# Optimization experiments

Hardware: AMD Instinct MI355X
Metric: run time of the kernel (lower is better)

Reference implementation:

```python
import jax, jax.numpy as jnp
import numpy as np

B, N = 8, 2048
IN_F, MID1, HID, MID2, OUT_F = 128, 128, 128, 128, 128
BIG = 9e15  # matches torch's 9000000000000000.0 additive mask constant


def _linear_params(key, out_d, in_d):
    # torch Linear layout: W is [out, in]
    kw, kb = jax.random.split(key)
    w = jax.random.normal(kw, (out_d, in_d), jnp.float32) * (1.0 / np.sqrt(in_d))
    b = jax.random.normal(kb, (out_d,), jnp.float32) * 0.01
    return w, b


def setup_inputs() -> dict:
    key = jax.random.key(0)
    ks = jax.random.split(key, 16)
    h = jax.random.normal(ks[0], (B, N, IN_F), jnp.float32)
    adj = jax.random.randint(ks[1], (B, N, N), 0, 2).astype(jnp.float32)
    vae2_fetures = jax.random.normal(ks[2], (B, N, OUT_F), jnp.float32)
    Wv1, bv1 = _linear_params(ks[3], MID1, IN_F)
    Wk1, bk1 = _linear_params(ks[4], MID1, IN_F)
    Wq1, bq1 = _linear_params(ks[5], MID1, IN_F)
    Wo1, bo1 = _linear_params(ks[6], HID, MID1)
    Wv2, bv2 = _linear_params(ks[7], MID2, HID)
    Wk2, bk2 = _linear_params(ks[8], MID2, HID)
    Wq2, bq2 = _linear_params(ks[9], MID2, HID)
    Wo2, bo2 = _linear_params(ks[10], OUT_F, MID2)
    Wf, bf = _linear_params(ks[11], OUT_F, 2 * OUT_F)
    return {
        "h": h, "adj": adj, "vae2_fetures": vae2_fetures,
        "Wv1": Wv1, "bv1": bv1, "Wk1": Wk1, "bk1": bk1, "Wq1": Wq1, "bq1": bq1,
        "Wo1": Wo1, "bo1": bo1,
        "Wv2": Wv2, "bv2": bv2, "Wk2": Wk2, "bk2": bk2, "Wq2": Wq2, "bq2": bq2,
        "Wo2": Wo2, "bo2": bo2, "Wf": Wf, "bf": bf,
    }


def _lin(x, W, b):
    return jnp.einsum('bnd,od->bno', x, W) + b


def _masked_att_block(x, adj, Wq, bq, Wk, bk, Wv, bv):
    v = jax.nn.relu(_lin(x, Wv, bv))          # [B,N,D]
    q = jax.nn.relu(_lin(x, Wq, bq))          # [B,N,D]
    k = jax.nn.relu(_lin(x, Wk, bk))          # [B,N,D]
    s = jnp.einsum('bnd,bmd->bnm', q, k)       # [B,N,N]
    masked = s * adj - BIG * (1.0 - adj)       # multiplicative + additive mask
    att = jax.nn.softmax(masked, axis=-1)
    return jnp.einsum('bnm,bmd->bnd', att, v)


def reference(h, adj, vae2_fetures,
              Wv1, bv1, Wk1, bk1, Wq1, bq1, Wo1, bo1,
              Wv2, bv2, Wk2, bk2, Wq2, bq2, Wo2, bo2,
              Wf, bf):
    f1 = _masked_att_block(h, adj, Wq1, bq1, Wk1, bk1, Wv1, bv1)
    f1 = _lin(f1, Wo1, bo1)                    # [B,N,HID]
    f2 = _masked_att_block(f1, adj, Wq2, bq2, Wk2, bk2, Wv2, bv2)
    f2 = _lin(f2, Wo2, bo2)                    # [B,N,OUT_F]
    f3 = jnp.concatenate([f2, vae2_fetures], axis=2)
    return _lin(f3, Wf, bf)                    # [B,N,OUT_F]
```

## Files before the change

### kernel.cpp

```cpp
#include <hip/hip_runtime.h>

typedef short s16x8 __attribute__((ext_vector_type(8)));
typedef float f32x4 __attribute__((ext_vector_type(4)));
typedef unsigned short u16x4v __attribute__((ext_vector_type(4)));

#define NSPLIT 4
#define NROWS 16384
#define MSHIFT 44.0f
#define NCH (2048 / NSPLIT / 64)

__device__ __forceinline__ unsigned short f2bf(float f) {
  union { float fl; unsigned int i; } v; v.fl = f;
  unsigned int x = v.i;
  x += 0x7fffu + ((x >> 16) & 1u);
  return (unsigned short)(x >> 16);
}
__device__ __forceinline__ s16x8 load8_bf16(const unsigned short* p) {
  return *(const s16x8*)p;
}
__device__ __forceinline__ s16x8 load8_f32(const float* p) {
  float4 a = *(const float4*)p;
  float4 b = *(const float4*)(p + 4);
  s16x8 r;
  r[0] = (short)f2bf(a.x); r[1] = (short)f2bf(a.y);
  r[2] = (short)f2bf(a.z); r[3] = (short)f2bf(a.w);
  r[4] = (short)f2bf(b.x); r[5] = (short)f2bf(b.y);
  r[6] = (short)f2bf(b.z); r[7] = (short)f2bf(b.w);
  return r;
}
__device__ __forceinline__ int vperm(int nn) {
  return (nn & ~31) | (((nn >> 2) & 3) << 3) | (((nn >> 4) & 1) << 2);
}

__device__ __forceinline__ void gload16(const void* g, void* l) {
  __builtin_amdgcn_global_load_lds(
      (const __attribute__((address_space(1))) void*)g,
      (__attribute__((address_space(3))) void*)l, 16, 0, 0);
}

__device__ __forceinline__ void pack_adj_body(
    const float* __restrict__ ADJ, unsigned long long* __restrict__ MASK)
{
  const int t = threadIdx.x;
  const int w = t >> 6;
  const int lane = t & 63;
  const int row0 = blockIdx.x * 16 + w * 4;
#pragma unroll
  for (int rr = 0; rr < 4; ++rr) {
    const float* src = ADJ + (size_t)(row0 + rr) * 2048;
    unsigned long long* dst = MASK + (size_t)(row0 + rr) * 32;
#pragma unroll 8
    for (int p = 0; p < 32; ++p) {
      const float v = src[p * 64 + lane];
      const unsigned long long word = __ballot(v != 0.f);
      if (lane == 0) dst[p] = word;
    }
  }
}

__device__ __forceinline__ void qkv_merged_body(
    const float* __restrict__ X,
    const float* __restrict__ Wq, const float* __restrict__ bq, unsigned short* __restrict__ oq,
    const float* __restrict__ Wk, const float* __restrict__ bk, unsigned short* __restrict__ ok,
    const float* __restrict__ Wv, const float* __restrict__ bv, unsigned short* __restrict__ ovt)
{
  const int t = threadIdx.x;
  const int w = t >> 6;
  const int lane = t & 63;
  const int l15 = lane & 15;
  const int quad = lane >> 4;
  const int mbase = blockIdx.x * 16;

  s16x8 a[4];
  const float* ar = X + (size_t)(mbase + l15) * 128;
#pragma unroll
  for (int ks = 0; ks < 4; ++ks) a[ks] = load8_f32(ar + ks * 32 + quad * 8);

  const float* Ws[3] = {Wq, Wk, Wv};
  const float* bs[3] = {bq, bk, bv};
  unsigned short* outs[3] = {oq, ok, ovt};

#pragma unroll
  for (int which = 0; which < 3; ++which) {
    const float* W = Ws[which];
    const float* bias = bs[which];
    unsigned short* out = outs[which];
#pragma unroll
    for (int nt = 0; nt < 2; ++nt) {
      const int n = (w * 2 + nt) * 16 + l15;
      f32x4 acc = {0.f, 0.f, 0.f, 0.f};
      const float* wr = W + (size_t)n * 128;
#pragma unroll
      for (int ks = 0; ks < 4; ++ks)
        acc = __builtin_amdgcn_mfma_f32_16x16x32_bf16(
            a[ks], load8_f32(wr + ks * 32 + quad * 8), acc, 0, 0, 0);
      const float bv_ = bias[n];
      if (which < 2) {
#pragma unroll
        for (int r = 0; r < 4; ++r)
          out[(size_t)(mbase + quad * 4 + r) * 128 + n] = f2bf(fmaxf(acc[r] + bv_, 0.f));
      } else {
        const int b  = mbase >> 11;
        const int nn = (mbase & 2047) + quad * 4;
        u16x4v pk;
#pragma unroll
        for (int r = 0; r < 4; ++r) pk[r] = f2bf(fmaxf(acc[r] + bv_, 0.f));
        *(u16x4v*)(out + (size_t)(b * 128 + n) * 2048 + vperm(nn)) = pk;
      }
    }
  }
}

__global__ __launch_bounds__(256) void qkv1_kernel(
    const float* __restrict__ x,
    const float* __restrict__ Wq, const float* __restrict__ bq, unsigned short* __restrict__ oq,
    const float* __restrict__ Wk, const float* __restrict__ bk, unsigned short* __restrict__ ok,
    const float* __restrict__ Wv, const float* __restrict__ bv, unsigned short* __restrict__ ovt,
    const float* __restrict__ adj, unsigned long long* __restrict__ mask)
{
  if (blockIdx.y == 0) qkv_merged_body(x, Wq, bq, oq, Wk, bk, ok, Wv, bv, ovt);
  else                 pack_adj_body(adj, mask);
}

__global__ __launch_bounds__(256, 2) void attn_kernel(
    const unsigned short* __restrict__ Q,
    const unsigned short* __restrict__ K,
    const unsigned short* __restrict__ VT,
    const unsigned long long* __restrict__ MASK,
    float* __restrict__ pO, float* __restrict__ pl)
{
  __shared__ __align__(16) unsigned short kbuf[2][64][128];
  __shared__ __align__(16) unsigned short vbuf[2][128][64];

  const int t = threadIdx.x;
  const int w = t >> 6;
  const int lane = t & 63;
  const int l15 = lane & 15;
  const int quad = lane >> 4;
  const int x7 = l15 & 7;

  const int gq0 = blockIdx.x * 128;
  const int b   = gq0 >> 11;
  const int wq0 = (gq0 & 2047) + w * 32;
  const int kc0 = blockIdx.y * (2048 / NSPLIT);

  const unsigned short* Kb  = K  + (size_t)(b * 2048) * 128;
  const unsigned short* VTb = VT + (size_t)(b * 128) * 2048;
  const unsigned long long* Mb = MASK + (size_t)b * 2048 * 32;

  const int krow = t >> 4;
  const int kc16 = t & 15;
  const int kchunk = kc16 ^ (krow & 7);
  const int vrow = t >> 3;
  const int vc16 = t & 7;
  const int vchunk = vc16 ^ (vrow & 7);

  s16x8 qf[2][4];
#pragma unroll
  for (int mt = 0; mt < 2; ++mt) {
    const unsigned short* qrow = Q + (size_t)(gq0 + w * 32 + mt * 16 + l15) * 128;
#pragma unroll
    for (int ks = 0; ks < 4; ++ks) qf[mt][ks] = load8_bf16(qrow + ks * 32 + quad * 8);
  }

  s16x8 ones;
#pragma unroll
  for (int i = 0; i < 8; ++i) ones[i] = (short)0x3F80;

  f32x4 accO[2][8];
  f32x4 accL[2];
#pragma unroll
  for (int mt = 0; mt < 2; ++mt) {
    accL[mt] = (f32x4){0.f, 0.f, 0.f, 0.f};
#pragma unroll
    for (int dt = 0; dt < 8; ++dt) accO[mt][dt] = (f32x4){0.f, 0.f, 0.f, 0.f};
  }

#pragma unroll
  for (int i = 0; i < 4; ++i)
    gload16(Kb + (size_t)(kc0 + i * 16 + krow) * 128 + kchunk * 8,
            &kbuf[0][i * 16 + krow][kc16 * 8]);
#pragma unroll
  for (int i = 0; i < 4; ++i)
    gload16(VTb + (size_t)(i * 32 + vrow) * 2048 + kc0 + vchunk * 8,
            &vbuf[0][i * 32 + vrow][vc16 * 8]);

  unsigned long long mwc[2];
#pragma unroll
  for (int mt = 0; mt < 2; ++mt)
    mwc[mt] = Mb[(size_t)(wq0 + mt * 16 + l15) * 32 + (kc0 >> 6)];

  __syncthreads();

#pragma unroll 2
  for (int ci = 0; ci < NCH; ++ci) {
    const int kc = kc0 + ci * 64;
    unsigned short (*kb)[128] = kbuf[ci & 1];
    unsigned short (*vb)[64]  = vbuf[ci & 1];

    if (ci + 1 < NCH) {
      unsigned short (*kbn)[128] = kbuf[(ci + 1) & 1];
      unsigned short (*vbn)[64]  = vbuf[(ci + 1) & 1];
#pragma unroll
      for (int i = 0; i < 4; ++i)
        gload16(Kb + (size_t)(kc + 64 + i * 16 + krow) * 128 + kchunk * 8,
                &kbn[i * 16 + krow][kc16 * 8]);
#pragma unroll
      for (int i = 0; i < 4; ++i)
        gload16(VTb + (size_t)(i * 32 + vrow) * 2048 + (kc + 64) + vchunk * 8,
                &vbn[i * 32 + vrow][vc16 * 8]);
    }

    unsigned long long kept[2];
    kept[0] = mwc[0];
    kept[1] = mwc[1];
    if (ci + 1 < NCH) {
#pragma unroll
      for (int mt = 0; mt < 2; ++mt)
        mwc[mt] = Mb[(size_t)(wq0 + mt * 16 + l15) * 32 + ((kc + 64) >> 6)];
    }

    f32x4 sv[2][4];
#pragma unroll
    for (int nt = 0; nt < 4; ++nt) {
      sv[0][nt] = (f32x4){0.f, 0.f, 0.f, 0.f};
      sv[1][nt] = (f32x4){0.f, 0.f, 0.f, 0.f};
    }
    __builtin_amdgcn_s_setprio(1);
#pragma unroll
    for (int nt = 0; nt < 4; ++nt)
#pragma unroll
      for (int ks = 0; ks < 4; ++ks) {
        s16x8 kf = *(const s16x8*)&kb[nt * 16 + l15][((ks * 4 + quad) ^ x7) * 8];
        sv[0][nt] = __builtin_amdgcn_mfma_f32_16x16x32_bf16(kf, qf[0][ks], sv[0][nt], 0, 0, 0);
        sv[1][nt] = __builtin_amdgcn_mfma_f32_16x16x32_bf16(kf, qf[1][ks], sv[1][nt], 0, 0, 0);
      }
    __builtin_amdgcn_s_setprio(0);

    s16x8 pf[2][2];
#pragma unroll
    for (int mt = 0; mt < 2; ++mt) {
      const unsigned int bl = (unsigned int)(kept[mt] >> (quad * 4));
      const unsigned int bh = (unsigned int)(kept[mt] >> (quad * 4 + 32));
#pragma unroll
      for (int ks = 0; ks < 2; ++ks) {
        s16x8 v;
#pragma unroll
        for (int half = 0; half < 2; ++half) {
          const int nt = ks * 2 + half;
          const unsigned int bits = (nt < 2) ? bl : bh;
          const int sh = (nt & 1) * 16;
#pragma unroll
          for (int r = 0; r < 4; ++r) {
            const float e = __expf(sv[mt][nt][r] - MSHIFT);
            const bool keep = (bits >> (sh + r)) & 1u;
            v[half * 4 + r] = (short)f2bf(keep ? e : 0.f);
          }
        }
        pf[mt][ks] = v;
      }
    }

    __builtin_amdgcn_s_setprio(1);
#pragma unroll
    for (int mt = 0; mt < 2; ++mt)
#pragma unroll
      for (int ks = 0; ks < 2; ++ks)
        accL[mt] = __builtin_amdgcn_mfma_f32_16x16x32_bf16(ones, pf[mt][ks], accL[mt], 0, 0, 0);

#pragma unroll
    for (int dt = 0; dt < 8; ++dt)
#pragma unroll
      for (int ks = 0; ks < 2; ++ks) {
        s16x8 vf = *(const s16x8*)&vb[dt * 16 + l15][((ks * 4 + quad) ^ x7) * 8];
        accO[0][dt] = __builtin_amdgcn_mfma_f32_16x16x32_bf16(vf, pf[0][ks], accO[0][dt], 0, 0, 0);
        accO[1][dt] = __builtin_amdgcn_mfma_f32_16x16x32_bf16(vf, pf[1][ks], accO[1][dt], 0, 0, 0);
      }
    __builtin_amdgcn_s_setprio(0);

    __syncthreads();
  }

  float* pOs = pO + (size_t)blockIdx.y * NROWS * 128;
#pragma unroll
  for (int mt = 0; mt < 2; ++mt) {
    const int qg = gq0 + w * 32 + mt * 16 + l15;
#pragma unroll
    for (int dt = 0; dt < 8; ++dt)
      *(f32x4*)(pOs + (size_t)qg * 128 + dt * 16 + quad * 4) = accO[mt][dt];
  }
  if (quad == 0) {
#pragma unroll
    for (int mt = 0; mt < 2; ++mt)
      pl[blockIdx.y * NROWS + gq0 + w * 32 + mt * 16 + l15] = accL[mt][0];
  }
}

__device__ __forceinline__ void combine64(
    const float* __restrict__ pO, const float* __restrict__ pl, int grow0,
    unsigned short (*At)[136])
{
  const int t = threadIdx.x;
#pragma unroll
  for (int u = 0; u < 4; ++u) {
    const int unit = u * 256 + t;
    const int row = unit >> 4;
    const int col8 = (unit & 15) * 8;
    const int grow = grow0 + row;
    float lsum = 0.f;
#pragma unroll
    for (int s = 0; s < NSPLIT; ++s) lsum += pl[s * NROWS + grow];
    const float inv = (lsum > 0.f) ? 1.f / lsum : 0.f;
    float acc8[8];
#pragma unroll
    for (int i = 0; i < 8; ++i) acc8[i] = 0.f;
#pragma unroll
    for (int s = 0; s < NSPLIT; ++s) {
      const float* p = pO + (size_t)s * NROWS * 128 + (size_t)grow * 128 + col8;
      float4 x0 = *(const float4*)p;
      float4 x1 = *(const float4*)(p + 4);
      acc8[0] += x0.x; acc8[1] += x0.y; acc8[2] += x0.z; acc8[3] += x0.w;
      acc8[4] += x1.x; acc8[5] += x1.y; acc8[6] += x1.z; acc8[7] += x1.w;
    }
#pragma unroll
    for (int i = 0; i < 8; ++i) At[row][col8 + i] = f2bf(acc8[i] * inv);
  }
}

__global__ __launch_bounds__(256) void redqkv_kernel(
    const float* __restrict__ pO, const float* __restrict__ pl,
    const float* __restrict__ Wo, const float* __restrict__ bo,
    const float* __restrict__ Wq, const float* __restrict__ bq, unsigned short* __restrict__ oq,
    const float* __restrict__ Wk, const float* __restrict__ bk, unsigned short* __restrict__ ok,
    const float* __restrict__ Wv, const float* __restrict__ bv, unsigned short* __restrict__ ovt)
{
  __shared__ __align__(16) unsigned short At[64][136];
  __shared__ __align__(16) unsigned short Bt[64][136];
  const int t = threadIdx.x;
  const int grow0 = blockIdx.x * 64;

  combine64(pO, pl, grow0, At);
  __syncthreads();

  const int w = t >> 6;
  const int lane = t & 63;
  const int l15 = lane & 15;
  const int quad = lane >> 4;

  s16x8 af[4][4];
#pragma unroll
  for (int mt = 0; mt < 4; ++mt)
#pragma unroll
    for (int ks = 0; ks < 4; ++ks)
      af[mt][ks] = *(const s16x8*)&At[mt * 16 + l15][ks * 32 + quad * 8];

#pragma unroll
  for (int nt = 0; nt < 2; ++nt) {
    const int n = (w * 2 + nt) * 16 + l15;
    const float* wr = Wo + (size_t)n * 128;
    s16x8 wf[4];
#pragma unroll
    for (int ks = 0; ks < 4; ++ks) wf[ks] = load8_f32(wr + ks * 32 + quad * 8);
    f32x4 acc[4];
#pragma unroll
    for (int mt = 0; mt < 4; ++mt) acc[mt] = (f32x4){0.f, 0.f, 0.f, 0.f};
#pragma unroll
    for (int mt = 0; mt < 4; ++mt)
#pragma unroll
      for (int ks = 0; ks < 4; ++ks)
        acc[mt] = __builtin_amdgcn_mfma_f32_16x16x32_bf16(af[mt][ks], wf[ks], acc[mt], 0, 0, 0);
    const float bv_ = bo[n];
#pragma unroll
    for (int mt = 0; mt < 4; ++mt)
#pragma unroll
      for (int r = 0; r < 4; ++r)
        Bt[mt * 16 + quad * 4 + r][n] = f2bf(acc[mt][r] + bv_);
  }
  __syncthreads();

  s16x8 a2[4][4];
#pragma unroll
  for (int mt = 0; mt < 4; ++mt)
#pragma unroll
    for (int ks = 0; ks < 4; ++ks)
      a2[mt][ks] = *(const s16x8*)&Bt[mt * 16 + l15][ks * 32 + quad * 8];

#pragma unroll
  for (int which = 0; which < 3; ++which) {
    const float* W = (which == 0) ? Wq : (which == 1) ? Wk : Wv;
    const float* bb = (which == 0) ? bq : (which == 1) ? bk : bv;
    unsigned short* out = (which == 0) ? oq : (which == 1) ? ok : ovt;
#pragma unroll
    for (int nt = 0; nt < 2; ++nt) {
      const int n = (w * 2 + nt) * 16 + l15;
      const float* wr = W + (size_t)n * 128;
      s16x8 wf[4];
#pragma unroll
      for (int ks = 0; ks < 4; ++ks) wf[ks] = load8_f32(wr + ks * 32 + quad * 8);
      f32x4 acc[4];
#pragma unroll
      for (int mt = 0; mt < 4; ++mt) acc[mt] = (f32x4){0.f, 0.f, 0.f, 0.f};
#pragma unroll
      for (int mt = 0; mt < 4; ++mt)
#pragma unroll
        for (int ks = 0; ks < 4; ++ks)
          acc[mt] = __builtin_amdgcn_mfma_f32_16x16x32_bf16(a2[mt][ks], wf[ks], acc[mt], 0, 0, 0);
      const float bv_ = bb[n];
      if (which < 2) {
#pragma unroll
        for (int mt = 0; mt < 4; ++mt)
#pragma unroll
          for (int r = 0; r < 4; ++r)
            out[(size_t)(grow0 + mt * 16 + quad * 4 + r) * 128 + n] =
                f2bf(fmaxf(acc[mt][r] + bv_, 0.f));
      } else {
        const int b = grow0 >> 11;
#pragma unroll
        for (int mt = 0; mt < 4; ++mt) {
          const int nn = (grow0 & 2047) + mt * 16 + quad * 4;
          u16x4v pk;
#pragma unroll
          for (int r = 0; r < 4; ++r) pk[r] = f2bf(fmaxf(acc[mt][r] + bv_, 0.f));
          *(u16x4v*)(out + (size_t)(b * 128 + n) * 2048 + vperm(nn)) = pk;
        }
      }
    }
  }
}

__global__ __launch_bounds__(256) void redfinal_kernel(
    const float* __restrict__ pO, const float* __restrict__ pl,
    const float* __restrict__ Wo, const float* __restrict__ bo,
    const float* __restrict__ Wf, const float* __restrict__ bff,
    const float* __restrict__ vae2, float* __restrict__ out)
{
  __shared__ __align__(16) unsigned short At[64][136];
  __shared__ __align__(16) unsigned short Bt[64][136];
  const int t = threadIdx.x;
  const int grow0 = blockIdx.x * 64;

  combine64(pO, pl, grow0, At);
  __syncthreads();

  const int w = t >> 6;
  const int lane = t & 63;
  const int l15 = lane & 15;
  const int quad = lane >> 4;

  s16x8 af[4][4];
#pragma unroll
  for (int mt = 0; mt < 4; ++mt)
#pragma unroll
    for (int ks = 0; ks < 4; ++ks)
      af[mt][ks] = *(const s16x8*)&At[mt * 16 + l15][ks * 32 + quad * 8];

#pragma unroll
  for (int nt = 0; nt < 2; ++nt) {
    const int n = (w * 2 + nt) * 16 + l15;
    const float* wr = Wo + (size_t)n * 128;
    s16x8 wf[4];
#pragma unroll
    for (int ks = 0; ks < 4; ++ks) wf[ks] = load8_f32(wr + ks * 32 + quad * 8);
    f32x4 acc[4];
#pragma unroll
    for (int mt = 0; mt < 4; ++mt) acc[mt] = (f32x4){0.f, 0.f, 0.f, 0.f};
#pragma unroll
    for (int mt = 0; mt < 4; ++mt)
#pragma unroll
      for (int ks = 0; ks < 4; ++ks)
        acc[mt] = __builtin_amdgcn_mfma_f32_16x16x32_bf16(af[mt][ks], wf[ks], acc[mt], 0, 0, 0);
    const float bv_ = bo[n];
#pragma unroll
    for (int mt = 0; mt < 4; ++mt)
#pragma unroll
      for (int r = 0; r < 4; ++r)
        Bt[mt * 16 + quad * 4 + r][n] = f2bf(acc[mt][r] + bv_);
  }
  __syncthreads();

  s16x8 a1[4][4], a2[4][4];
#pragma unroll
  for (int mt = 0; mt < 4; ++mt) {
#pragma unroll
    for (int ks = 0; ks < 4; ++ks)
      a1[mt][ks] = *(const s16x8*)&Bt[mt * 16 + l15][ks * 32 + quad * 8];
    const float* vrow = vae2 + (size_t)(grow0 + mt * 16 + l15) * 128;
#pragma unroll
    for (int ks = 0; ks < 4; ++ks) a2[mt][ks] = load8_f32(vrow + ks * 32 + quad * 8);
  }

#pragma unroll
  for (int nt = 0; nt < 2; ++nt) {
    const int n = (w * 2 + nt) * 16 + l15;
    const float* wr = Wf + (size_t)n * 256;
    s16x8 wfl[4], wfr[4];
#pragma unroll
    for (int ks = 0; ks < 4; ++ks) {
      wfl[ks] = load8_f32(wr + ks * 32 + quad * 8);
      wfr[ks] = load8_f32(wr + 128 + ks * 32 + quad * 8);
    }
    f32x4 acc[4];
#pragma unroll
    for (int mt = 0; mt < 4; ++mt) acc[mt] = (f32x4){0.f, 0.f, 0.f, 0.f};
#pragma unroll
    for (int mt = 0; mt < 4; ++mt) {
#pragma unroll
      for (int ks = 0; ks < 4; ++ks)
        acc[mt] = __builtin_amdgcn_mfma_f32_16x16x32_bf16(a1[mt][ks], wfl[ks], acc[mt], 0, 0, 0);
#pragma unroll
      for (int ks = 0; ks < 4; ++ks)
        acc[mt] = __builtin_amdgcn_mfma_f32_16x16x32_bf16(a2[mt][ks], wfr[ks], acc[mt], 0, 0, 0);
    }
    const float bv_ = bff[n];
#pragma unroll
    for (int mt = 0; mt < 4; ++mt)
#pragma unroll
      for (int r = 0; r < 4; ++r)
        out[(size_t)(grow0 + mt * 16 + quad * 4 + r) * 128 + n] = acc[mt][r] + bv_;
  }
}

extern "C" void kernel_launch(void* const* d_in, const int* in_sizes, int n_in,
                              void* d_out, int out_size, void* d_ws, size_t ws_size,
                              hipStream_t stream)
{
  const float* h    = (const float*)d_in[0];
  const float* adj  = (const float*)d_in[1];
  const float* vae2 = (const float*)d_in[2];
  const float* Wv1  = (const float*)d_in[3];
  const float* bv1  = (const float*)d_in[4];
  const float* Wk1  = (const float*)d_in[5];
  const float* bk1  = (const float*)d_in[6];
  const float* Wq1  = (const float*)d_in[7];
  const float* bq1  = (const float*)d_in[8];
  const float* Wo1  = (const float*)d_in[9];
  const float* bo1  = (const float*)d_in[10];
  const float* Wv2  = (const float*)d_in[11];
  const float* bv2  = (const float*)d_in[12];
  const float* Wk2  = (const float*)d_in[13];
  const float* bk2  = (const float*)d_in[14];
  const float* Wq2  = (const float*)d_in[15];
  const float* bq2  = (const float*)d_in[16];
  const float* Wo2  = (const float*)d_in[17];
  const float* bo2  = (const float*)d_in[18];
  const float* Wf   = (const float*)d_in[19];
  const float* bff  = (const float*)d_in[20];

  char* wsb = (char*)d_ws;
  const size_t MB = 1u << 20;
  unsigned short* s_q  = (unsigned short*)(wsb + 0 * MB);
  unsigned short* s_k  = (unsigned short*)(wsb + 4 * MB);
  unsigned short* s_vt = (unsigned short*)(wsb + 8 * MB);
  unsigned long long* maskp = (unsigned long long*)(wsb + 12 * MB);
  float* pO = (float*)(wsb + 16 * MB);
  float* pl = (float*)(wsb + 48 * MB);

  qkv1_kernel<<<dim3(1024, 2), dim3(256), 0, stream>>>(
      h, Wq1, bq1, s_q, Wk1, bk1, s_k, Wv1, bv1, s_vt, adj, maskp);
  attn_kernel<<<dim3(128, NSPLIT), dim3(256), 0, stream>>>(
      s_q, s_k, s_vt, maskp, pO, pl);
  redqkv_kernel<<<dim3(256), dim3(256), 0, stream>>>(
      pO, pl, Wo1, bo1, Wq2, bq2, s_q, Wk2, bk2, s_k, Wv2, bv2, s_vt);
  attn_kernel<<<dim3(128, NSPLIT), dim3(256), 0, stream>>>(
      s_q, s_k, s_vt, maskp, pO, pl);
  redfinal_kernel<<<dim3(256), dim3(256), 0, stream>>>(
      pO, pl, Wo2, bo2, Wf, bff, vae2, (float*)d_out);
}
```

Measured before the change: 391.6 us.

## Repack adjacency mask layout and batch mask loads; widen QKV row tiles

The adjacency packer now reads float4 per lane and ballots each component, producing a permuted bit layout written as 32 words per row by one wave. The attention kernel loads four mask words per 256-key group with 128-bit loads instead of one scalar word per chunk, and decodes bits with the new interleaved layout. The QKV projection handles 64 rows per block, reusing each converted weight fragment across four row tiles. This cuts mask load instructions and redundant weight conversion, at the cost of more registers and a more intricate mask decoding that must match the packer exactly.

New measurement: 355.0 us. 1.1x faster.

```diff
diff --git a/kernel.cpp b/kernel.cpp
--- a/kernel.cpp
+++ b/kernel.cpp
@@ -39,23 +39,33 @@
 }
 
 __device__ __forceinline__ void pack_adj_body(
-    const float* __restrict__ ADJ, unsigned long long* __restrict__ MASK)
+    const float* __restrict__ ADJ, unsigned long long* __restrict__ MASK,
+    int pblk)
 {
   const int t = threadIdx.x;
   const int w = t >> 6;
   const int lane = t & 63;
-  const int row0 = blockIdx.x * 16 + w * 4;
-#pragma unroll
-  for (int rr = 0; rr < 4; ++rr) {
-    const float* src = ADJ + (size_t)(row0 + rr) * 2048;
-    unsigned long long* dst = MASK + (size_t)(row0 + rr) * 32;
-#pragma unroll 8
-    for (int p = 0; p < 32; ++p) {
-      const float v = src[p * 64 + lane];
-      const unsigned long long word = __ballot(v != 0.f);
-      if (lane == 0) dst[p] = word;
-    }
-  }
+  const int row = pblk * 4 + w;
+
+  const float4* src = (const float4*)(ADJ + (size_t)row * 2048);
+  float4 v[8];
+#pragma unroll
+  for (int j = 0; j < 8; ++j) v[j] = src[j * 64 + lane];
+
+  unsigned long long wm = 0ull;
+#pragma unroll
+  for (int j = 0; j < 8; ++j) {
+    const unsigned long long b0 = __ballot(v[j].x != 0.f);
+    wm = (lane == j * 4 + 0) ? b0 : wm;
+    const unsigned long long b1 = __ballot(v[j].y != 0.f);
+    wm = (lane == j * 4 + 1) ? b1 : wm;
+    const unsigned long long b2 = __ballot(v[j].z != 0.f);
+    wm = (lane == j * 4 + 2) ? b2 : wm;
+    const unsigned long long b3 = __ballot(v[j].w != 0.f);
+    wm = (lane == j * 4 + 3) ? b3 : wm;
+  }
+
+  if (lane < 32) MASK[(size_t)row * 32 + lane] = wm;
 }
 
 __device__ __forceinline__ void qkv_merged_body(
@@ -69,12 +79,15 @@
   const int lane = t & 63;
   const int l15 = lane & 15;
   const int quad = lane >> 4;
-  const int mbase = blockIdx.x * 16;
-
-  s16x8 a[4];
-  const float* ar = X + (size_t)(mbase + l15) * 128;
-#pragma unroll
-  for (int ks = 0; ks < 4; ++ks) a[ks] = load8_f32(ar + ks * 32 + quad * 8);
+  const int mbase = blockIdx.x * 64;
+
+  s16x8 af[4][4];
+#pragma unroll
+  for (int mt = 0; mt < 4; ++mt) {
+    const float* ar = X + (size_t)(mbase + mt * 16 + l15) * 128;
+#pragma unroll
+    for (int ks = 0; ks < 4; ++ks) af[mt][ks] = load8_f32(ar + ks * 32 + quad * 8);
+  }
 
   const float* Ws[3] = {Wq, Wk, Wv};
   const float* bs[3] = {bq, bk, bv};
@@ -88,24 +101,36 @@
 #pragma unroll
     for (int nt = 0; nt < 2; ++nt) {
       const int n = (w * 2 + nt) * 16 + l15;
-      f32x4 acc = {0.f, 0.f, 0.f, 0.f};
       const float* wr = W + (size_t)n * 128;
-#pragma unroll
-      for (int ks = 0; ks < 4; ++ks)
-        acc = __builtin_amdgcn_mfma_f32_16x16x32_bf16(
-            a[ks], load8_f32(wr + ks * 32 + quad * 8), acc, 0, 0, 0);
+      s16x8 wf[4];
+#pragma unroll
+      for (int ks = 0; ks < 4; ++ks) wf[ks] = load8_f32(wr + ks * 32 + quad * 8);
+      f32x4 acc[4];
+#pragma unroll
+      for (int mt = 0; mt < 4; ++mt) acc[mt] = (f32x4){0.f, 0.f, 0.f, 0.f};
+#pragma unroll
+      for (int mt = 0; mt < 4; ++mt)
+#pragma unroll
+        for (int ks = 0; ks < 4; ++ks)
+          acc[mt] = __builtin_amdgcn_mfma_f32_16x16x32_bf16(af[mt][ks], wf[ks], acc[mt], 0, 0, 0);
       const float bv_ = bias[n];
       if (which < 2) {
 #pragma unroll
-        for (int r = 0; r < 4; ++r)
-          out[(size_t)(mbase + quad * 4 + r) * 128 + n] = f2bf(fmaxf(acc[r] + bv_, 0.f));
+        for (int mt = 0; mt < 4; ++mt)
+#pragma unroll
+          for (int r = 0; r < 4; ++r)
+            out[(size_t)(mbase + mt * 16 + quad * 4 + r) * 128 + n] =
+                f2bf(fmaxf(acc[mt][r] + bv_, 0.f));
       } else {
-        const int b  = mbase >> 11;
-        const int nn = (mbase & 2047) + quad * 4;
-        u16x4v pk;
-#pragma unroll
-        for (int r = 0; r < 4; ++r) pk[r] = f2bf(fmaxf(acc[r] + bv_, 0.f));
-        *(u16x4v*)(out + (size_t)(b * 128 + n) * 2048 + vperm(nn)) = pk;
+        const int b = mbase >> 11;
+#pragma unroll
+        for (int mt = 0; mt < 4; ++mt) {
+          const int nn = (mbase & 2047) + mt * 16 + quad * 4;
+          u16x4v pk;
+#pragma unroll
+          for (int r = 0; r < 4; ++r) pk[r] = f2bf(fmaxf(acc[mt][r] + bv_, 0.f));
+          *(u16x4v*)(out + (size_t)(b * 128 + n) * 2048 + vperm(nn)) = pk;
+        }
       }
     }
   }
@@ -118,8 +143,8 @@
     const float* __restrict__ Wv, const float* __restrict__ bv, unsigned short* __restrict__ ovt,
     const float* __restrict__ adj, unsigned long long* __restrict__ mask)
 {
-  if (blockIdx.y == 0) qkv_merged_body(x, Wq, bq, oq, Wk, bk, ok, Wv, bv, ovt);
-  else                 pack_adj_body(adj, mask);
+  if (blockIdx.x < 256) qkv_merged_body(x, Wq, bq, oq, Wk, bk, ok, Wv, bv, ovt);
+  else                  pack_adj_body(adj, mask, blockIdx.x - 256);
 }
 
 __global__ __launch_bounds__(256, 2) void attn_kernel(
@@ -185,100 +210,99 @@
     gload16(VTb + (size_t)(i * 32 + vrow) * 2048 + kc0 + vchunk * 8,
             &vbuf[0][i * 32 + vrow][vc16 * 8]);
 
-  unsigned long long mwc[2];
-#pragma unroll
-  for (int mt = 0; mt < 2; ++mt)
-    mwc[mt] = Mb[(size_t)(wq0 + mt * 16 + l15) * 32 + (kc0 >> 6)];
-
   __syncthreads();
 
-#pragma unroll 2
-  for (int ci = 0; ci < NCH; ++ci) {
-    const int kc = kc0 + ci * 64;
-    unsigned short (*kb)[128] = kbuf[ci & 1];
-    unsigned short (*vb)[64]  = vbuf[ci & 1];
-
-    if (ci + 1 < NCH) {
-      unsigned short (*kbn)[128] = kbuf[(ci + 1) & 1];
-      unsigned short (*vbn)[64]  = vbuf[(ci + 1) & 1];
-#pragma unroll
-      for (int i = 0; i < 4; ++i)
-        gload16(Kb + (size_t)(kc + 64 + i * 16 + krow) * 128 + kchunk * 8,
-                &kbn[i * 16 + krow][kc16 * 8]);
-#pragma unroll
-      for (int i = 0; i < 4; ++i)
-        gload16(VTb + (size_t)(i * 32 + vrow) * 2048 + (kc + 64) + vchunk * 8,
-                &vbn[i * 32 + vrow][vc16 * 8]);
-    }
-
-    unsigned long long kept[2];
-    kept[0] = mwc[0];
-    kept[1] = mwc[1];
-    if (ci + 1 < NCH) {
+  for (int g = 0; g < 2; ++g) {
+    const int jj = (kc0 >> 8) + g;
+    ulonglong2 m01[2], m23[2];
+#pragma unroll
+    for (int mt = 0; mt < 2; ++mt) {
+      const unsigned long long* mrow = Mb + (size_t)(wq0 + mt * 16 + l15) * 32 + jj * 4;
+      m01[mt] = *(const ulonglong2*)mrow;
+      m23[mt] = *(const ulonglong2*)(mrow + 2);
+    }
+
+#pragma unroll
+    for (int cg = 0; cg < 4; ++cg) {
+      const int kc = kc0 + g * 256 + cg * 64;
+      unsigned short (*kb)[128] = kbuf[cg & 1];
+      unsigned short (*vb)[64]  = vbuf[cg & 1];
+
+      if (g == 0 || cg < 3) {
+        unsigned short (*kbn)[128] = kbuf[(cg + 1) & 1];
+        unsigned short (*vbn)[64]  = vbuf[(cg + 1) & 1];
+#pragma unroll
+        for (int i = 0; i < 4; ++i)
+          gload16(Kb + (size_t)(kc + 64 + i * 16 + krow) * 128 + kchunk * 8,
+                  &kbn[i * 16 + krow][kc16 * 8]);
+#pragma unroll
+        for (int i = 0; i < 4; ++i)
+          gload16(VTb + (size_t)(i * 32 + vrow) * 2048 + (kc + 64) + vchunk * 8,
+                  &vbn[i * 32 + vrow][vc16 * 8]);
+      }
+
+      f32x4 sv[2][4];
+#pragma unroll
+      for (int nt = 0; nt < 4; ++nt) {
+        sv[0][nt] = (f32x4){0.f, 0.f, 0.f, 0.f};
+        sv[1][nt] = (f32x4){0.f, 0.f, 0.f, 0.f};
+      }
+      __builtin_amdgcn_s_setprio(1);
+#pragma unroll
+      for (int nt = 0; nt < 4; ++nt)
+#pragma unroll
+        for (int ks = 0; ks < 4; ++ks) {
+          s16x8 kf = *(const s16x8*)&kb[nt * 16 + l15][((ks * 4 + quad) ^ x7) * 8];
+          sv[0][nt] = __builtin_amdgcn_mfma_f32_16x16x32_bf16(kf, qf[0][ks], sv[0][nt], 0, 0, 0);
+          sv[1][nt] = __builtin_amdgcn_mfma_f32_16x16x32_bf16(kf, qf[1][ks], sv[1][nt], 0, 0, 0);
+        }
+      __builtin_amdgcn_s_setprio(0);
+
+      s16x8 pf[2][2];
+#pragma unroll
+      for (int mt = 0; mt < 2; ++mt) {
+        const unsigned long long bse0 = m01[mt].x >> (cg * 16 + quad);
+        const unsigned long long bse1 = m01[mt].y >> (cg * 16 + quad);
+        const unsigned long long bse2 = m23[mt].x >> (cg * 16 + quad);
+        const unsigned long long bse3 = m23[mt].y >> (cg * 16 + quad);
+#pragma unroll
+        for (int ks = 0; ks < 2; ++ks) {
+          s16x8 v;
+#pragma unroll
+          for (int half = 0; half < 2; ++half) {
+            const int nt = ks * 2 + half;
+#pragma unroll
+            for (int r = 0; r < 4; ++r) {
+              const float e = __expf(sv[mt][nt][r] - MSHIFT);
+              const unsigned long long bw = (r == 0) ? bse0 : (r == 1) ? bse1
+                                          : (r == 2) ? bse2 : bse3;
+              const bool keep = (bw >> (nt * 4)) & 1ull;
+              v[half * 4 + r] = (short)f2bf(keep ? e : 0.f);
+            }
+          }
+          pf[mt][ks] = v;
+        }
+      }
+
+      __builtin_amdgcn_s_setprio(1);
 #pragma unroll
       for (int mt = 0; mt < 2; ++mt)
-        mwc[mt] = Mb[(size_t)(wq0 + mt * 16 + l15) * 32 + ((kc + 64) >> 6)];
-    }
-
-    f32x4 sv[2][4];
-#pragma unroll
-    for (int nt = 0; nt < 4; ++nt) {
-      sv[0][nt] = (f32x4){0.f, 0.f, 0.f, 0.f};
-      sv[1][nt] = (f32x4){0.f, 0.f, 0.f, 0.f};
-    }
-    __builtin_amdgcn_s_setprio(1);
-#pragma unroll
-    for (int nt = 0; nt < 4; ++nt)
-#pragma unroll
-      for (int ks = 0; ks < 4; ++ks) {
-        s16x8 kf = *(const s16x8*)&kb[nt * 16 + l15][((ks * 4 + quad) ^ x7) * 8];
-        sv[0][nt] = __builtin_amdgcn_mfma_f32_16x16x32_bf16(kf, qf[0][ks], sv[0][nt], 0, 0, 0);
-        sv[1][nt] = __builtin_amdgcn_mfma_f32_16x16x32_bf16(kf, qf[1][ks], sv[1][nt], 0, 0, 0);
-      }
-    __builtin_amdgcn_s_setprio(0);
-
-    s16x8 pf[2][2];
-#pragma unroll
-    for (int mt = 0; mt < 2; ++mt) {
-      const unsigned int bl = (unsigned int)(kept[mt] >> (quad * 4));
-      const unsigned int bh = (unsigned int)(kept[mt] >> (quad * 4 + 32));
-#pragma unroll
-      for (int ks = 0; ks < 2; ++ks) {
-        s16x8 v;
-#pragma unroll
-        for (int half = 0; half < 2; ++half) {
-          const int nt = ks * 2 + half;
-          const unsigned int bits = (nt < 2) ? bl : bh;
-          const int sh = (nt & 1) * 16;
-#pragma unroll
-          for (int r = 0; r < 4; ++r) {
-            const float e = __expf(sv[mt][nt][r] - MSHIFT);
-            const bool keep = (bits >> (sh + r)) & 1u;
-            v[half * 4 + r] = (short)f2bf(keep ? e : 0.f);
-          }
+#pragma unroll
+        for (int ks = 0; ks < 2; ++ks)
+          accL[mt] = __builtin_amdgcn_mfma_f32_16x16x32_bf16(ones, pf[mt][ks], accL[mt], 0, 0, 0);
+
+#pragma unroll
+      for (int dt = 0; dt < 8; ++dt)
+#pragma unroll
+        for (int ks = 0; ks < 2; ++ks) {
+          s16x8 vf = *(const s16x8*)&vb[dt * 16 + l15][((ks * 4 + quad) ^ x7) * 8];
+          accO[0][dt] = __builtin_amdgcn_mfma_f32_16x16x32_bf16(vf, pf[0][ks], accO[0][dt], 0, 0, 0);
+          accO[1][dt] = __builtin_amdgcn_mfma_f32_16x16x32_bf16(vf, pf[1][ks], accO[1][dt], 0, 0, 0);
         }
-        pf[mt][ks] = v;
-      }
-    }
-
-    __builtin_amdgcn_s_setprio(1);
-#pragma unroll
-    for (int mt = 0; mt < 2; ++mt)
-#pragma unroll
-      for (int ks = 0; ks < 2; ++ks)
-        accL[mt] = __builtin_amdgcn_mfma_f32_16x16x32_bf16(ones, pf[mt][ks], accL[mt], 0, 0, 0);
-
-#pragma unroll
-    for (int dt = 0; dt < 8; ++dt)
-#pragma unroll
-      for (int ks = 0; ks < 2; ++ks) {
-        s16x8 vf = *(const s16x8*)&vb[dt * 16 + l15][((ks * 4 + quad) ^ x7) * 8];
-        accO[0][dt] = __builtin_amdgcn_mfma_f32_16x16x32_bf16(vf, pf[0][ks], accO[0][dt], 0, 0, 0);
-        accO[1][dt] = __builtin_amdgcn_mfma_f32_16x16x32_bf16(vf, pf[1][ks], accO[1][dt], 0, 0, 0);
-      }
-    __builtin_amdgcn_s_setprio(0);
-
-    __syncthreads();
+      __builtin_amdgcn_s_setprio(0);
+
+      __syncthreads();
+    }
   }
 
   float* pOs = pO + (size_t)blockIdx.y * NROWS * 128;
@@ -555,7 +579,7 @@
   float* pO = (float*)(wsb + 16 * MB);
   float* pl = (float*)(wsb + 48 * MB);
 
-  qkv1_kernel<<<dim3(1024, 2), dim3(256), 0, stream>>>(
+  qkv1_kernel<<<dim3(256 + 4096), dim3(256), 0, stream>>>(
       h, Wq1, bq1, s_q, Wk1, bk1, s_k, Wv1, bv1, s_vt, adj, maskp);
   attn_kernel<<<dim3(128, NSPLIT), dim3(256), 0, stream>>>(
       s_q, s_k, s_vt, maskp, pO, pl);
```
